# Kernel tuning notes

Hardware: AMD Instinct MI355X
Metric: run time of the kernel (lower is better)

## Reference

```python
import jax, jax.numpy as jnp
import numpy as np

N_GENES = 2048   # col_dim: nodes of the PPI graph, feature dim of cols-SAGE
N_CELLS = 4096   # row_dim: nodes of the KNN graph, feature dim of rows-SAGE
E_KNN = 61440
E_PPI = 65536
INTER = 512
EMBD = 128
SLOPE = 0.01       # LeakyReLU default negative_slope
SCALE_PARAM = 3.0  # cols_encoder custom attention scale

_PARAM_SHAPES = [
    ("c0_wl", (N_GENES, N_GENES)), ("c0_wr", (N_GENES, N_GENES)), ("c0_b", (N_GENES,)),
    ("r0_wl", (N_CELLS, N_CELLS)), ("r0_wr", (N_CELLS, N_CELLS)), ("r0_b", (N_CELLS,)),
    ("c1_wl", (N_GENES, N_GENES)), ("c1_wr", (N_GENES, N_GENES)), ("c1_b", (N_GENES,)),
    ("r1_wl", (N_CELLS, N_CELLS)), ("r1_wr", (N_CELLS, N_CELLS)), ("r1_b", (N_CELLS,)),
    ("gr_w", (N_CELLS, INTER)), ("gr_b", (INTER,)),
    ("tr_wq", (INTER, EMBD)), ("tr_bq", (EMBD,)), ("tr_wk", (INTER, EMBD)), ("tr_bk", (EMBD,)),
    ("tr_wv", (INTER, EMBD)), ("tr_bv", (EMBD,)), ("tr_ws", (INTER, EMBD)), ("tr_bs", (EMBD,)),
    ("gc_w", (N_GENES, INTER)), ("gc_b", (INTER,)),
    ("tc_wq", (INTER, EMBD)), ("tc_bq", (EMBD,)), ("tc_wk", (INTER, EMBD)), ("tc_bk", (EMBD,)),
    ("tc_wv", (INTER, EMBD)), ("tc_bv", (EMBD,)), ("tc_ws", (INTER, EMBD)), ("tc_bs", (EMBD,)),
    ("d1_w", (EMBD, INTER)), ("d1_b", (INTER,)),
    ("d2_w", (INTER, INTER)), ("d2_b", (INTER,)),
    ("d3_w", (INTER, N_GENES)), ("d3_b", (N_GENES,)),
]


def setup_inputs() -> dict:
    key = jax.random.key(0)
    ki = iter(jax.random.split(key, 64))
    inp = {
        "x": jax.random.normal(next(ki), (N_GENES, N_CELLS), jnp.float32),
        "knn_edge_index": jax.random.randint(next(ki), (2, E_KNN), 0, N_CELLS, dtype=jnp.int32),
        "ppi_edge_index": jax.random.randint(next(ki), (2, E_PPI), 0, N_GENES, dtype=jnp.int32),
    }
    for name, shape in _PARAM_SHAPES:
        scale = 1.0 / float(np.sqrt(shape[0])) if len(shape) == 2 else 0.01
        inp[name] = jax.random.normal(next(ki), shape, jnp.float32) * scale
    return inp


def _leaky(x):
    return jax.nn.leaky_relu(x, SLOPE)


def _gcn(x, ei, w, b):
    # GCNConv: add self loops, symmetric D^-1/2 (A+I) D^-1/2 normalization
    n = x.shape[0]
    loop = jnp.arange(n, dtype=ei.dtype)
    src = jnp.concatenate([ei[0], loop])
    dst = jnp.concatenate([ei[1], loop])
    deg = jax.ops.segment_sum(jnp.ones(src.shape, x.dtype), dst, n)
    dinv = jnp.where(deg > 0, jax.lax.rsqrt(jnp.maximum(deg, 1.0)), 0.0)
    h = x @ w
    msg = h[src] * (dinv[src] * dinv[dst])[:, None]
    return jax.ops.segment_sum(msg, dst, n) + b


def _sage(x, ei, wl, wr, b):
    # SAGEConv: mean neighbor aggregation -> lin_l, plus root lin_r
    n = x.shape[0]
    src, dst = ei[0], ei[1]
    s = jax.ops.segment_sum(x[src], dst, n)
    cnt = jax.ops.segment_sum(jnp.ones(src.shape, x.dtype), dst, n)
    agg = s / jnp.maximum(cnt, 1.0)[:, None]
    return agg @ wl + x @ wr + b


def _tconv(x, ei, wq, bq, wk, bk, wv, bv, ws, bs, scale_param):
    # TransformerConv (heads=1). scale_param=None -> per-target softmax;
    # otherwise the custom mean/std standardization + sigmoid (TransformerConvReducrLayer).
    n, d = x.shape[0], wq.shape[1]
    q = x @ wq + bq
    k = x @ wk + bk
    v = x @ wv + bv
    src, dst = ei[0], ei[1]
    alpha = jnp.sum(q[dst] * k[src], axis=-1) / jnp.sqrt(jnp.asarray(d, x.dtype))
    if scale_param is None:
        m = jax.ops.segment_max(alpha, dst, n)
        e = jnp.exp(alpha - m[dst])
        z = jax.ops.segment_sum(e, dst, n)
        a = e / jnp.where(z > 0, z, 1.0)[dst]
    else:
        mu = jnp.mean(alpha)
        sd = jnp.std(alpha, ddof=1)  # torch.std is unbiased
        a = jax.nn.sigmoid((alpha - mu) / ((1.0 / scale_param) * sd))
    out = jax.ops.segment_sum(a[:, None] * v[src], dst, n)
    return out + x @ ws + bs  # root skip (lin_skip)


def reference(x, knn_edge_index, ppi_edge_index,
              c0_wl, c0_wr, c0_b, r0_wl, r0_wr, r0_b,
              c1_wl, c1_wr, c1_b, r1_wl, r1_wr, r1_b,
              gr_w, gr_b, tr_wq, tr_bq, tr_wk, tr_bk, tr_wv, tr_bv, tr_ws, tr_bs,
              gc_w, gc_b, tc_wq, tc_bq, tc_wk, tc_bk, tc_wv, tc_bv, tc_ws, tc_bs,
              d1_w, d1_b, d2_w, d2_b, d3_w, d3_b):
    # dropout layers are identity at inference
    emb = x  # [genes, cells]
    for (cwl, cwr, cb, rwl, rwr, rb) in [
        (c0_wl, c0_wr, c0_b, r0_wl, r0_wr, r0_b),
        (c1_wl, c1_wr, c1_b, r1_wl, r1_wr, r1_b),
    ]:
        emb = _leaky(_sage(emb.T, knn_edge_index, cwl, cwr, cb)).T  # cells graph
        emb = _leaky(_sage(emb, ppi_edge_index, rwl, rwr, rb))      # genes graph
    # rows encoder: GCN + TransformerConv (softmax attention) over PPI graph
    hr = _leaky(_gcn(emb, ppi_edge_index, gr_w, gr_b))
    emb_rows = _tconv(hr, ppi_edge_index, tr_wq, tr_bq, tr_wk, tr_bk,
                      tr_wv, tr_bv, tr_ws, tr_bs, None)
    # cols encoder: GCN + reducer TransformerConv (sigmoid-standardized attention) over KNN graph
    hc = _leaky(_gcn(emb.T, knn_edge_index, gc_w, gc_b))
    emb_cols = _tconv(hc, knn_edge_index, tc_wq, tc_bq, tc_wk, tc_bk,
                      tc_wv, tc_bv, tc_ws, tc_bs, SCALE_PARAM)
    # feature decoder MLP
    h = jax.nn.relu(emb_cols @ d1_w + d1_b)
    h = jax.nn.relu(h @ d2_w + d2_b)
    out_features = h @ d3_w + d3_b
    return (emb_rows, emb_cols, out_features)
```

## Files before the change

kernel.cpp:

```cpp
#include <hip/hip_runtime.h>
#include <math.h>

#define NG 2048
#define NC 4096
#define EKNN 61440
#define EPPI 65536

typedef __attribute__((ext_vector_type(8))) short short8v;
typedef __attribute__((ext_vector_type(4))) float f32x4;
typedef unsigned short ushort_t;

static inline int cdiv(int a, int b) { return (a + b - 1) / b; }

__device__ __forceinline__ unsigned short f2b(float f) {
    union { float f; unsigned int i; } v; v.f = f;
    unsigned int r = v.i + 0x7FFFu + ((v.i >> 16) & 1u);
    return (unsigned short)(r >> 16);
}
__device__ __forceinline__ float bl(unsigned int u) { union { unsigned int i; float f; } v; v.i = u << 16; return v.f; }
__device__ __forceinline__ float bh(unsigned int u) { union { unsigned int i; float f; } v; v.i = u & 0xFFFF0000u; return v.f; }
__device__ __forceinline__ unsigned int pk2(float a, float b) { return (unsigned int)f2b(a) | ((unsigned int)f2b(b) << 16); }

__device__ __forceinline__ int xcd_swz_id() {
    const int nwg = gridDim.x * gridDim.y;
    const int orig = blockIdx.y * gridDim.x + blockIdx.x;
    const int q = nwg >> 3, r = nwg & 7;
    const int xcd = orig & 7, off = orig >> 3;
    return (xcd < r ? xcd * (q + 1) : r * (q + 1) + (xcd - r) * q) + off;
}

#define GLOAD_LDS16(gp, lp) __builtin_amdgcn_global_load_lds( \
    (const __attribute__((address_space(1))) void*)(gp),      \
    (__attribute__((address_space(3))) void*)(lp), 16, 0, 0)

template<int ACT, bool BIAS, bool OBF>
__global__ __launch_bounds__(256)
void gemm_bf16(const ushort_t* __restrict__ A,
               const ushort_t* __restrict__ Bt,
               const float* __restrict__ bias,
               float* __restrict__ Cf, ushort_t* __restrict__ Cb,
               int M, int N, int K) {
    __shared__ ushort_t lds[2][2][128 * 32];
    const int tid = threadIdx.x;
    const int lane = tid & 63, wv = tid >> 6;
    const int wm = wv >> 1, wn = wv & 1;
    const int swzid = xcd_swz_id();
    const int bm = (swzid / gridDim.x) << 7, bn = (swzid % gridDim.x) << 7;

    const ushort_t* gA = A + (size_t)bm * K;
    const ushort_t* gB = Bt + (size_t)bn * K;
    const int rsub = lane >> 2;
    const int qsw  = (lane & 3) ^ ((lane >> 3) & 3);
    const int KT = K >> 5;

    f32x4 acc[4][4];
    #pragma unroll
    for (int i = 0; i < 4; ++i)
        #pragma unroll
        for (int j = 0; j < 4; ++j) acc[i][j] = (f32x4){0.f, 0.f, 0.f, 0.f};

    auto stage = [&](int buf, int k0) {
        #pragma unroll
        for (int t = 0; t < 2; ++t) {
            const int br = (wv * 2 + t) * 16;
            GLOAD_LDS16(gA + (size_t)(br + rsub) * K + k0 + qsw * 8, &lds[buf][0][br * 32]);
            GLOAD_LDS16(gB + (size_t)(br + rsub) * K + k0 + qsw * 8, &lds[buf][1][br * 32]);
        }
    };
    const int rl = lane & 15, kg = lane >> 4;
    const int swr = (kg ^ ((rl >> 1) & 3)) * 8;

    stage(0, 0);
    int buf = 0;
    for (int kt = 0; kt < KT; ++kt) {
        __syncthreads();
        if (kt + 1 < KT) stage(buf ^ 1, (kt + 1) << 5);
        short8v a[4], b[4];
        #pragma unroll
        for (int mi = 0; mi < 4; ++mi)
            a[mi] = *(const short8v*)&lds[buf][0][(wm * 64 + mi * 16 + rl) * 32 + swr];
        #pragma unroll
        for (int ni = 0; ni < 4; ++ni)
            b[ni] = *(const short8v*)&lds[buf][1][(wn * 64 + ni * 16 + rl) * 32 + swr];
        #pragma unroll
        for (int mi = 0; mi < 4; ++mi)
            #pragma unroll
            for (int ni = 0; ni < 4; ++ni)
                acc[mi][ni] = __builtin_amdgcn_mfma_f32_16x16x32_bf16(a[mi], b[ni], acc[mi][ni], 0, 0, 0);
        buf ^= 1;
    }
    const int colL = lane & 15, rq = lane >> 4;
    #pragma unroll
    for (int mi = 0; mi < 4; ++mi) {
        const int row0 = bm + wm * 64 + mi * 16 + rq * 4;
        #pragma unroll
        for (int ni = 0; ni < 4; ++ni) {
            const int col = bn + wn * 64 + ni * 16 + colL;
            float bv = 0.f;
            if (BIAS) bv = bias[col];
            #pragma unroll
            for (int r = 0; r < 4; ++r) {
                const size_t off = (size_t)(row0 + r) * N + col;
                float v = acc[mi][ni][r];
                if (BIAS) v += bv;
                if (ACT == 2) v = fmaxf(v, 0.f);
                if (OBF) Cb[off] = f2b(v); else Cf[off] = v;
            }
        }
    }
}

template<bool BIAS, bool OBF>
__global__ __launch_bounds__(256)
void gemm2_bf16(const ushort_t* __restrict__ A0, const ushort_t* __restrict__ Bt0,
                const float* __restrict__ bias0, float* __restrict__ Cf0, ushort_t* __restrict__ Cb0,
                int N0, int K0, int nx0, int nb0,
// ... 80 lines not shown
}

__global__ __launch_bounds__(256)
void gemm_sage(const ushort_t* __restrict__ A0, const ushort_t* __restrict__ B0t,
               const ushort_t* __restrict__ A1, const ushort_t* __restrict__ B1t,
               const float* __restrict__ bias, ushort_t* __restrict__ Cb,
               int M, int N, int K) {
    __shared__ ushort_t lds[2][2][128 * 32];
    const int tid = threadIdx.x;
    const int lane = tid & 63, wv = tid >> 6;
    const int wm = wv >> 1, wn = wv & 1;
    const int swzid = xcd_swz_id();
    const int bm = (swzid / gridDim.x) << 7, bn = (swzid % gridDim.x) << 7;

    const ushort_t* gA0 = A0 + (size_t)bm * K;
    const ushort_t* gB0 = B0t + (size_t)bn * K;
    const ushort_t* gA1 = A1 + (size_t)bm * K;
    const ushort_t* gB1 = B1t + (size_t)bn * K;
    const int rsub = lane >> 2;
    const int qsw  = (lane & 3) ^ ((lane >> 3) & 3);
    const int KT = K >> 5;

    f32x4 acc[4][4];
    #pragma unroll
    for (int i = 0; i < 4; ++i)
        #pragma unroll
        for (int j = 0; j < 4; ++j) acc[i][j] = (f32x4){0.f, 0.f, 0.f, 0.f};

    auto stage = [&](int buf, int kt) {
        const int half = kt >= KT;
        const int k0 = (half ? (kt - KT) : kt) << 5;
        const ushort_t* sA = half ? gA1 : gA0;
        const ushort_t* sB = half ? gB1 : gB0;
        #pragma unroll
        for (int t = 0; t < 2; ++t) {
            const int br = (wv * 2 + t) * 16;
            GLOAD_LDS16(sA + (size_t)(br + rsub) * K + k0 + qsw * 8, &lds[buf][0][br * 32]);
            GLOAD_LDS16(sB + (size_t)(br + rsub) * K + k0 + qsw * 8, &lds[buf][1][br * 32]);
        }
    };
    const int rl = lane & 15, kg = lane >> 4;
    const int swr = (kg ^ ((rl >> 1) & 3)) * 8;

    stage(0, 0);
    int buf = 0;
    const int KT2 = KT * 2;
    for (int kt = 0; kt < KT2; ++kt) {
        __syncthreads();
        if (kt + 1 < KT2) stage(buf ^ 1, kt + 1);
        short8v a[4], b[4];
        #pragma unroll
        for (int mi = 0; mi < 4; ++mi)
            a[mi] = *(const short8v*)&lds[buf][0][(wm * 64 + mi * 16 + rl) * 32 + swr];
        #pragma unroll
        for (int ni = 0; ni < 4; ++ni)
            b[ni] = *(const short8v*)&lds[buf][1][(wn * 64 + ni * 16 + rl) * 32 + swr];
        #pragma unroll
        for (int mi = 0; mi < 4; ++mi)
            #pragma unroll
            for (int ni = 0; ni < 4; ++ni)
                acc[mi][ni] = __builtin_amdgcn_mfma_f32_16x16x32_bf16(a[mi], b[ni], acc[mi][ni], 0, 0, 0);
        buf ^= 1;
    }
    const int colL = lane & 15, rq = lane >> 4;
    #pragma unroll
    for (int mi = 0; mi < 4; ++mi) {
        const int row0 = bm + wm * 64 + mi * 16 + rq * 4;
        float bz[4];
        #pragma unroll
        for (int r = 0; r < 4; ++r) bz[r] = bias[row0 + r];
        #pragma unroll
        for (int ni = 0; ni < 4; ++ni) {
            const int col = bn + wn * 64 + ni * 16 + colL;
            #pragma unroll
            for (int r = 0; r < 4; ++r) {
                float v = acc[mi][ni][r] + bz[r];
                v = v > 0.f ? v : 0.01f * v;
                Cb[(size_t)(row0 + r) * N + col] = f2b(v);
            }
        }
    }
}

__global__ __launch_bounds__(256)
void transpose_f2b(const float* __restrict__ in, ushort_t* __restrict__ out, int R, int C) {
    __shared__ ushort_t t[64][65];
    const int bx = blockIdx.x << 6, by = blockIdx.y << 6;
    const int tr = threadIdx.x >> 4;
    const int tc = (threadIdx.x & 15) << 2;
    #pragma unroll
    for (int i = 0; i < 4; ++i) {
        const int rr = tr + i * 16;
        const float4 v = *(const float4*)(in + (size_t)(by + rr) * C + bx + tc);
        t[rr][tc + 0] = f2b(v.x); t[rr][tc + 1] = f2b(v.y);
        t[rr][tc + 2] = f2b(v.z); t[rr][tc + 3] = f2b(v.w);
    }
    __syncthreads();
    #pragma unroll
    for (int i = 0; i < 4; ++i) {
        const int cc = tr + i * 16;
        ushort4 o;
        o.x = t[tc + 0][cc]; o.y = t[tc + 1][cc];
        o.z = t[tc + 2][cc]; o.w = t[tc + 3][cc];
        *(ushort4*)(out + (size_t)(bx + cc) * R + by + tc) = o;
    }
}

__global__ __launch_bounds__(256)
void transpose_f2b2(const float* __restrict__ in0, ushort_t* __restrict__ out0,
                    const float* __restrict__ in1, ushort_t* __restrict__ out1, int R, int C) {
    const float* in = blockIdx.z ? in1 : in0;
    ushort_t* out = blockIdx.z ? out1 : out0;
    __shared__ ushort_t t[64][65];
    const int bx = blockIdx.x << 6, by = blockIdx.y << 6;
    const int tr = threadIdx.x >> 4;
    const int tc = (threadIdx.x & 15) << 2;
    #pragma unroll
    for (int i = 0; i < 4; ++i) {
        const int rr = tr + i * 16;
        const float4 v = *(const float4*)(in + (size_t)(by + rr) * C + bx + tc);
        t[rr][tc + 0] = f2b(v.x); t[rr][tc + 1] = f2b(v.y);
        t[rr][tc + 2] = f2b(v.z); t[rr][tc + 3] = f2b(v.w);
    }
    __syncthreads();
    #pragma unroll
    for (int i = 0; i < 4; ++i) {
        const int cc = tr + i * 16;
        ushort4 o;
        o.x = t[tc + 0][cc]; o.y = t[tc + 1][cc];
        o.z = t[tc + 2][cc]; o.w = t[tc + 3][cc];
        *(ushort4*)(out + (size_t)(bx + cc) * R + by + tc) = o;
    }
}

__global__ __launch_bounds__(256)
void transpose_b2b(const ushort_t* __restrict__ in, ushort_t* __restrict__ out, int R, int C) {
    __shared__ ushort_t t[64][65];
    const int bx = blockIdx.x << 6, by = blockIdx.y << 6;
    const int tr = threadIdx.x >> 4;
    const int tc = (threadIdx.x & 15) << 2;
    #pragma unroll
    for (int i = 0; i < 4; ++i) {
        const int rr = tr + i * 16;
        const ushort4 v = *(const ushort4*)(in + (size_t)(by + rr) * C + bx + tc);
        t[rr][tc + 0] = v.x; t[rr][tc + 1] = v.y;
        t[rr][tc + 2] = v.z; t[rr][tc + 3] = v.w;
    }
    __syncthreads();
    #pragma unroll
    for (int i = 0; i < 4; ++i) {
        const int cc = tr + i * 16;
        ushort4 o;
        o.x = t[tc + 0][cc]; o.y = t[tc + 1][cc];
        o.z = t[tc + 2][cc]; o.w = t[tc + 3][cc];
        *(ushort4*)(out + (size_t)(bx + cc) * R + by + tc) = o;
    }
}

__global__ __launch_bounds__(256)
void transpose_qkvs8(const float* __restrict__ w0, const float* __restrict__ w1,
                     const float* __restrict__ w2, const float* __restrict__ w3,
                     const float* __restrict__ w4, const float* __restrict__ w5,
                     const float* __restrict__ w6, const float* __restrict__ w7,
                     ushort_t* __restrict__ outR, ushort_t* __restrict__ outC) {
    const int z = blockIdx.z;
    const float* in;
    switch (z) {
        case 0: in = w0; break; case 1: in = w1; break;
        case 2: in = w2; break; case 3: in = w3; break;
        case 4: in = w4; break; case 5: in = w5; break;
        case 6: in = w6; break; default: in = w7; break;
    }
    ushort_t* o = (z < 4 ? outR + (size_t)z * 128 * 512 : outC + (size_t)(z - 4) * 128 * 512);
    __shared__ ushort_t t[64][65];
    const int bx = blockIdx.x << 6, by = blockIdx.y << 6;
    const int tr = threadIdx.x >> 4;
    const int tc = (threadIdx.x & 15) << 2;
    #pragma unroll
    for (int i = 0; i < 4; ++i) {
        const int rr = tr + i * 16;
        const float4 v = *(const float4*)(in + (size_t)(by + rr) * 128 + bx + tc);
        t[rr][tc + 0] = f2b(v.x); t[rr][tc + 1] = f2b(v.y);
        t[rr][tc + 2] = f2b(v.z); t[rr][tc + 3] = f2b(v.w);
    }
    __syncthreads();
    #pragma unroll
    for (int i = 0; i < 4; ++i) {
        const int cc = tr + i * 16;
        ushort4 ov;
        ov.x = t[tc + 0][cc]; ov.y = t[tc + 1][cc];
        ov.z = t[tc + 2][cc]; ov.w = t[tc + 3][cc];
        *(ushort4*)(o + (size_t)(bx + cc) * 512 + by + tc) = ov;
    }
}

__global__ void count_dst2(const int* __restrict__ pdst, float* __restrict__ cntp,
                           const int* __restrict__ kdst, float* __restrict__ cntk) {
    int e = blockIdx.x * blockDim.x + threadIdx.x;
    if (e < EPPI) atomicAdd(&cntp[pdst[e]], 1.0f);
    else if (e < EPPI + EKNN) atomicAdd(&cntk[kdst[e - EPPI]], 1.0f);
}

__global__ void make_dinv2(const float* __restrict__ cntp, float* __restrict__ dinvp,
                           const float* __restrict__ cntk, float* __restrict__ dinvk) {
    int i = blockIdx.x * blockDim.x + threadIdx.x;
    if (i < NG) dinvp[i] = rsqrtf(cntp[i] + 1.0f);
    else if (i < NG + NC) dinvk[i - NG] = rsqrtf(cntk[i - NG] + 1.0f);
}

__global__ __launch_bounds__(256)
void scan_rowptr2(const float* __restrict__ cntp, int* __restrict__ rpp,
                  const float* __restrict__ cntk, int* __restrict__ rpk) {
    const float* cnt = blockIdx.x ? cntk : cntp;
    int* rowptr = blockIdx.x ? rpk : rpp;
    const int n = blockIdx.x ? NC : NG;
    __shared__ int part[257];
    const int tid = threadIdx.x;
    const int per = n >> 8;
    const int base = tid * per;
    int s = 0;
    for (int i = 0; i < per; ++i) s += (int)cnt[base + i];
    part[tid + 1] = s;
    if (tid == 0) part[0] = 0;
    __syncthreads();
    if (tid == 0)
        for (int i = 1; i <= 256; ++i) part[i] += part[i - 1];
    __syncthreads();
    int run = part[tid];
    for (int i = 0; i < per; ++i) {
        rowptr[base + i] = run;
        run += (int)cnt[base + i];
    }
    if (tid == 255) rowptr[n] = run;
}

__global__ void fill_csr2(const int* __restrict__ psrc, const int* __restrict__ pdst,
                          const int* __restrict__ rpp, int* __restrict__ curp,
                          int* __restrict__ srcp, int* __restrict__ eidp,
                          const int* __restrict__ ksrc, const int* __restrict__ kdst,
                          const int* __restrict__ rpk, int* __restrict__ curk,
                          int* __restrict__ srck, int* __restrict__ eidk) {
    int e = blockIdx.x * blockDim.x + threadIdx.x;
    if (e < EPPI) {
        int d = pdst[e];
        int p = atomicAdd(&curp[d], 1);
        srcp[rpp[d] + p] = psrc[e];
        eidp[rpp[d] + p] = e;
    } else if (e < EPPI + EKNN) {
        int e2 = e - EPPI;
        int d = kdst[e2];
        int p = atomicAdd(&curk[d], 1);
        srck[rpk[d] + p] = ksrc[e2];
        eidk[rpk[d] + p] = e2;
    }
}

__global__ void concat8(const float* __restrict__ a, const float* __restrict__ b,
                        const float* __restrict__ c, const float* __restrict__ d,
                        const float* __restrict__ e, const float* __restrict__ f,
                        const float* __restrict__ g, const float* __restrict__ h,
                        float* __restrict__ o) {
    int i = threadIdx.x + blockIdx.x * blockDim.x;
    if (i >= 1024) return;
    const float* s;
    int j = i & 127;
    switch (i >> 7) {
        case 0: s = a; break; case 1: s = b; break; case 2: s = c; break; case 3: s = d; break;
        case 4: s = e; break; case 5: s = f; break; case 6: s = g; break; default: s = h; break;
    }
    o[i] = s[j];
}

template<int NS>
__global__ __launch_bounds__(256)
void sage_gather_b(const int* __restrict__ rowptr, const int* __restrict__ srcs,
                   const ushort_t* __restrict__ x, ushort_t* __restrict__ out) {
    const int F = NS * 2048;
    const int node = blockIdx.x, tid = threadIdx.x;
    const int beg = rowptr[node], end = rowptr[node + 1];
    __shared__ int snb[256];
    float acc[NS][8];
    #pragma unroll
    for (int s = 0; s < NS; ++s)
        #pragma unroll
        for (int j = 0; j < 8; ++j) acc[s][j] = 0.f;
    for (int c = beg; c < end; c += 256) {
        const int m = min(256, end - c);
        __syncthreads();
        if (tid < m) snb[tid] = srcs[c + tid];
        __syncthreads();
        #pragma unroll 2
        for (int i = 0; i < m; ++i) {
            const uint4* row = (const uint4*)(x + (size_t)snb[i] * F);
            #pragma unroll
            for (int s = 0; s < NS; ++s) {
                const uint4 v = row[tid + s * 256];
                acc[s][0] += bl(v.x); acc[s][1] += bh(v.x);
                acc[s][2] += bl(v.y); acc[s][3] += bh(v.y);
                acc[s][4] += bl(v.z); acc[s][5] += bh(v.z);
                acc[s][6] += bl(v.w); acc[s][7] += bh(v.w);
            }
        }
    }
    const float inv = 1.f / fmaxf((float)(end - beg), 1.f);
    uint4* orow = (uint4*)(out + (size_t)node * F);
    #pragma unroll
    for (int s = 0; s < NS; ++s) {
        uint4 o;
        o.x = pk2(acc[s][0] * inv, acc[s][1] * inv);
        o.y = pk2(acc[s][2] * inv, acc[s][3] * inv);
        o.z = pk2(acc[s][4] * inv, acc[s][5] * inv);
        o.w = pk2(acc[s][6] * inv, acc[s][7] * inv);
        orow[tid + s * 256] = o;
    }
}

__global__ __launch_bounds__(128)
void gcn_gather2(const int* __restrict__ rpp, const int* __restrict__ srcp,
                 const ushort_t* __restrict__ hr, const float* __restrict__ dinvp,
                 const float* __restrict__ br, ushort_t* __restrict__ outr,
                 const int* __restrict__ rpk, const int* __restrict__ srck,
                 const ushort_t* __restrict__ hc, const float* __restrict__ dinvk,
                 const float* __restrict__ bc, ushort_t* __restrict__ outc) {
    const bool cols = blockIdx.x >= NG;
    const int node = cols ? blockIdx.x - NG : blockIdx.x;
    const int tid = threadIdx.x;
    const int* rowptr = cols ? rpk : rpp;
    const int* srcs = cols ? srck : srcp;
    const ushort_t* h = cols ? hc : hr;
    const float* dinv = cols ? dinvk : dinvp;
    const float* b = cols ? bc : br;
    ushort_t* out = cols ? outc : outr;

    const int beg = rowptr[node], end = rowptr[node + 1];
    __shared__ int snb[128];
    __shared__ float sdi[128];
    float ax = 0.f, ay = 0.f, az = 0.f, aw = 0.f;
    for (int c = beg; c < end; c += 128) {
        const int m = min(128, end - c);
        __syncthreads();
        if (tid < m) { int s = srcs[c + tid]; snb[tid] = s; sdi[tid] = dinv[s]; }
        __syncthreads();
        for (int i = 0; i < m; ++i) {
            const uint2 v = ((const uint2*)(h + (size_t)snb[i] * 512))[tid];
            const float w = sdi[i];
            ax += bl(v.x) * w; ay += bh(v.x) * w;
            az += bl(v.y) * w; aw += bh(v.y) * w;
        }
    }
    const float dd = dinv[node];
    const uint2 hv = ((const uint2*)(h + (size_t)node * 512))[tid];
    const float4 bv = ((const float4*)b)[tid];
    float4 o;
    o.x = ax * dd + bl(hv.x) * dd * dd + bv.x;
    o.y = ay * dd + bh(hv.x) * dd * dd + bv.y;
    o.z = az * dd + bl(hv.y) * dd * dd + bv.z;
    o.w = aw * dd + bh(hv.y) * dd * dd + bv.w;
    o.x = o.x > 0.f ? o.x : 0.01f * o.x;
    o.y = o.y > 0.f ? o.y : 0.01f * o.y;
    o.z = o.z > 0.f ? o.z : 0.01f * o.z;
    o.w = o.w > 0.f ? o.w : 0.01f * o.w;
    ((uint2*)(out + (size_t)node * 512))[tid] = make_uint2(pk2(o.x, o.y), pk2(o.z, o.w));
}

__global__ __launch_bounds__(256)
void edge_dot2(const int* __restrict__ psrc, const int* __restrict__ pdst,
               const float* __restrict__ qr, float* __restrict__ alphap,
               const int* __restrict__ ksrc, const int* __restrict__ kdst,
               const float* __restrict__ qc, float* __restrict__ alphak) {
    int wid = (blockIdx.x * blockDim.x + threadIdx.x) >> 6;
    int lane = threadIdx.x & 63;
    const float* q;
    float* out;
    int s, d, w;
    if (wid < EPPI) {
        w = wid; s = psrc[w]; d = pdst[w]; q = qr; out = alphap;
    } else if (wid < EPPI + EKNN) {
        w = wid - EPPI; s = ksrc[w]; d = kdst[w]; q = qc; out = alphak;
    } else return;
    const size_t qb = (size_t)d * 512;
    const size_t kb = (size_t)s * 512 + 128;
    float v = q[qb + lane] * q[kb + lane] + q[qb + 64 + lane] * q[kb + 64 + lane];
    #pragma unroll
    for (int off = 32; off; off >>= 1) v += __shfl_down(v, off);
    if (lane == 0) out[w] = v * 0.08838834764831845f;
}

__global__ __launch_bounds__(256)
void reduce_stats(const float* __restrict__ a, int E, double* __restrict__ stats) {
    double s = 0.0, s2 = 0.0;
    for (int i = blockIdx.x * blockDim.x + threadIdx.x; i < E; i += gridDim.x * blockDim.x) {
        double x = a[i];
        s += x; s2 += x * x;
    }
    #pragma unroll
    for (int off = 32; off; off >>= 1) {
        s += __shfl_down(s, off);
        s2 += __shfl_down(s2, off);
    }
    __shared__ double sh[4][2];
    int w = threadIdx.x >> 6;
    if ((threadIdx.x & 63) == 0) { sh[w][0] = s; sh[w][1] = s2; }
    __syncthreads();
    if (threadIdx.x == 0) {
        double t = sh[0][0] + sh[1][0] + sh[2][0] + sh[3][0];
        double t2 = sh[0][1] + sh[1][1] + sh[2][1] + sh[3][1];
        atomicAdd(&stats[0], t);
        atomicAdd(&stats[1], t2);
    }
}

__global__ __launch_bounds__(128)
void tconv2(const int* __restrict__ rpp, const int* __restrict__ srcp,
            const int* __restrict__ eidp, const float* __restrict__ alphap,
            const float* __restrict__ qr, float* __restrict__ outr,
            const int* __restrict__ rpk, const int* __restrict__ srck,
            const int* __restrict__ eidk, const float* __restrict__ alphak,
            const float* __restrict__ qc, const double* __restrict__ stats,
            float* __restrict__ outc, ushort_t* __restrict__ ob) {
    const int tid = threadIdx.x;
    __shared__ int snb[128];
    __shared__ float sa[128];
    if (blockIdx.x < NG) {
        const int node = blockIdx.x;
        const int beg = rpp[node], end = rpp[node + 1];
        float mx = -INFINITY;
        for (int c = beg; c < end; c += 128) {
            const int m = min(128, end - c);
            __syncthreads();
            if (tid < m) sa[tid] = alphap[eidp[c + tid]];
            __syncthreads();
            for (int i = 0; i < m; ++i) mx = fmaxf(mx, sa[i]);
        }
        float acc = 0.f, z = 0.f;
        for (int c = beg; c < end; c += 128) {
            const int m = min(128, end - c);
            __syncthreads();
            if (tid < m) { snb[tid] = srcp[c + tid]; sa[tid] = __expf(alphap[eidp[c + tid]] - mx); }
            __syncthreads();
            for (int i = 0; i < m; ++i) {
                z += sa[i];
                acc += sa[i] * qr[(size_t)snb[i] * 512 + 256 + tid];
            }
        }
        const float r = acc * (z > 0.f ? 1.f / z : 0.f) + qr[(size_t)node * 512 + 384 + tid];
        outr[(size_t)node * 128 + tid] = r;
    } else {
        const int node = blockIdx.x - NG;
        const int beg = rpk[node], end = rpk[node + 1];
        const double sum = stats[0], sumsq = stats[1];
        const double mu = sum / (double)EKNN;
        const double var = (sumsq - sum * sum / (double)EKNN) / (double)(EKNN - 1);
        const float sd = (float)sqrt(fmax(var, 0.0));
        const float kk = 3.0f / sd;
        const float fmu = (float)mu;
        float acc = 0.f;
        for (int c = beg; c < end; c += 128) {
            const int m = min(128, end - c);
            __syncthreads();
            if (tid < m) {
                snb[tid] = srck[c + tid];
                const float t = (alphak[eidk[c + tid]] - fmu) * kk;
                sa[tid] = 1.f / (1.f + __expf(-t));
            }
            __syncthreads();
            for (int i = 0; i < m; ++i)
                acc += sa[i] * qc[(size_t)snb[i] * 512 + 256 + tid];
        }
        const float r = acc + qc[(size_t)node * 512 + 384 + tid];
        outc[(size_t)node * 128 + tid] = r;
        ob[(size_t)node * 128 + tid] = f2b(r);
    }
}

static constexpr size_t NBIG = (size_t)NG * NC;
static constexpr size_t NBH = NBIG / 2;
static constexpr size_t OFF_B1 = 0;
static constexpr size_t OFF_B2 = NBH;
static constexpr size_t OFF_B3 = 2 * NBH;
static constexpr size_t OFF_WBF = 3 * NBH;
static constexpr size_t OFF_OV   = OFF_WBF + 2097152;
static constexpr size_t OFF_HRB  = OFF_OV;
static constexpr size_t OFF_HCB  = OFF_HRB + 524288;
static constexpr size_t OFF_H2B  = OFF_HCB + 1048576;
static constexpr size_t OFF_H3B  = OFF_H2B + 524288;
static constexpr size_t OFF_QKVSR = OFF_H3B + 1048576;
static constexpr size_t OFF_QKVSC = OFF_QKVSR + 1048576;
static constexpr size_t OFF_CBF  = OFF_QKVSC + 2097152;
static constexpr size_t OFF_WQR  = OFF_CBF + 262144;
static constexpr size_t OFF_WQC  = OFF_WQR + 131072;
static constexpr size_t OFF_D1T  = OFF_WQC + 131072;
static constexpr size_t OFF_D2T  = OFF_D1T + 32768;
static constexpr size_t OFF_D3T  = OFF_D2T + 131072;
static constexpr size_t OFF_TAIL = OFF_WBF + 2 * NBIG;
static constexpr size_t OFF_B4   = OFF_TAIL;
static constexpr size_t OFF_ALPHAP = OFF_B4 + 1024;
static constexpr size_t OFF_ALPHAK = OFF_ALPHAP + EPPI;
static constexpr size_t OFF_CNT  = OFF_ALPHAK + EKNN;
static constexpr size_t OFF_DINVP = OFF_CNT + 12288;
static constexpr size_t OFF_DINVK = OFF_DINVP + NG;
static constexpr size_t OFF_STATS = OFF_DINVK + NC;
static constexpr size_t OFF_RPP  = OFF_STATS + 16;
static constexpr size_t OFF_RPK  = OFF_RPP + 2064;
static constexpr size_t OFF_SRCP = OFF_RPK + 4112;
static constexpr size_t OFF_EIDP = OFF_SRCP + EPPI;
static constexpr size_t OFF_SRCK = OFF_EIDP + EPPI;
static constexpr size_t OFF_EIDK = OFF_SRCK + EKNN;

extern "C" void kernel_launch(void* const* d_in, const int* in_sizes, int n_in,
                              void* d_out, int out_size, void* d_ws, size_t ws_size,
                              hipStream_t stream) {
    const float* x      = (const float*)d_in[0];
    const int*   knn    = (const int*)d_in[1];
    const int*   ppi    = (const int*)d_in[2];
    const float* c0_wl = (const float*)d_in[3],  *c0_wr = (const float*)d_in[4],  *c0_b = (const float*)d_in[5];
    const float* r0_wl = (const float*)d_in[6],  *r0_wr = (const float*)d_in[7],  *r0_b = (const float*)d_in[8];
    const float* c1_wl = (const float*)d_in[9],  *c1_wr = (const float*)d_in[10], *c1_b = (const float*)d_in[11];
    const float* r1_wl = (const float*)d_in[12], *r1_wr = (const float*)d_in[13], *r1_b = (const float*)d_in[14];
    const float* gr_w  = (const float*)d_in[15], *gr_b  = (const float*)d_in[16];
    const float* tr_wq = (const float*)d_in[17], *tr_bq = (const float*)d_in[18];
    const float* tr_wk = (const float*)d_in[19], *tr_bk = (const float*)d_in[20];
    const float* tr_wv = (const float*)d_in[21], *tr_bv = (const float*)d_in[22];
    const float* tr_ws = (const float*)d_in[23], *tr_bs = (const float*)d_in[24];
    const float* gc_w  = (const float*)d_in[25], *gc_b  = (const float*)d_in[26];
    const float* tc_wq = (const float*)d_in[27], *tc_bq = (const float*)d_in[28];
    const float* tc_wk = (const float*)d_in[29], *tc_bk = (const float*)d_in[30];
    const float* tc_wv = (const float*)d_in[31], *tc_bv = (const float*)d_in[32];
    const float* tc_ws = (const float*)d_in[33], *tc_bs = (const float*)d_in[34];
    const float* d1_w  = (const float*)d_in[35], *d1_b  = (const float*)d_in[36];
    const float* d2_w  = (const float*)d_in[37], *d2_b  = (const float*)d_in[38];
    const float* d3_w  = (const float*)d_in[39], *d3_b  = (const float*)d_in[40];

    const int* knn_src = knn, *knn_dst = knn + EKNN;
    const int* ppi_src = ppi, *ppi_dst = ppi + EPPI;

    float* ws = (float*)d_ws;
    ushort_t* B1 = (ushort_t*)(ws + OFF_B1);
    ushort_t* B2 = (ushort_t*)(ws + OFF_B2);
    ushort_t* B3 = (ushort_t*)(ws + OFF_B3);
    ushort_t* WBF0 = (ushort_t*)(ws + OFF_WBF);
    ushort_t* WBF1 = WBF0 + 2 * NBIG;
    ushort_t* GRT = WBF0;
    ushort_t* GCT = WBF0 + 2097152;
    ushort_t* HRB = (ushort_t*)(ws + OFF_HRB);
    ushort_t* HCB = (ushort_t*)(ws + OFF_HCB);
    ushort_t* H2B = (ushort_t*)(ws + OFF_H2B);
    ushort_t* H3B = (ushort_t*)(ws + OFF_H3B);
    float* QKVSR = ws + OFF_QKVSR;
    float* QKVSC = ws + OFF_QKVSC;
    ushort_t* CBF = (ushort_t*)(ws + OFF_CBF);
    ushort_t* WQR = (ushort_t*)(ws + OFF_WQR);
    ushort_t* WQC = (ushort_t*)(ws + OFF_WQC);
    ushort_t* D1T = (ushort_t*)(ws + OFF_D1T);
    ushort_t* D2T = (ushort_t*)(ws + OFF_D2T);
    ushort_t* D3T = (ushort_t*)(ws + OFF_D3T);
    float* B4 = ws + OFF_B4;
    float* ALPHAP = ws + OFF_ALPHAP;
    float* ALPHAK = ws + OFF_ALPHAK;
    float* CNTP = ws + OFF_CNT;
    float* CNTK = CNTP + NG;
    int* CURP = (int*)(CNTK + NC);
    int* CURK = CURP + NG;
    float* DINVP = ws + OFF_DINVP;
    float* DINVK = ws + OFF_DINVK;
    double* STATS = (double*)(ws + OFF_STATS);
    int* RPP  = (int*)(ws + OFF_RPP);
    int* RPK  = (int*)(ws + OFF_RPK);
    int* SRCP = (int*)(ws + OFF_SRCP);
    int* EIDP = (int*)(ws + OFF_EIDP);
    int* SRCK = (int*)(ws + OFF_SRCK);
    int* EIDK = (int*)(ws + OFF_EIDK);

    float* out_rows = (float*)d_out;
    float* out_cols = out_rows + (size_t)NG * 128;
    float* out_feat = out_cols + (size_t)NC * 128;

    auto tW = [&](const float* Wsrc, int K, int N, ushort_t* dst) {
        transpose_f2b<<<dim3(N >> 6, K >> 6), 256, 0, stream>>>(Wsrc, dst, K, N);
    };
    auto gemm = [&](const ushort_t* Abf, const ushort_t* Wt, const float* bias,
                    float* Cf, ushort_t* Cb, int M, int N, int K, int mode) {
        dim3 g(N >> 7, M >> 7), blk(256);
        switch (mode) {
            case 2: gemm_bf16<0, true,  false><<<g, blk, 0, stream>>>(Abf, Wt, bias, Cf, nullptr, M, N, K); break;
            case 3: gemm_bf16<2, true,  true ><<<g, blk, 0, stream>>>(Abf, Wt, bias, nullptr, Cb, M, N, K); break;
        }
    };

    hipMemsetAsync(CNTP, 0, 12288 * 4, stream);
    count_dst2<<<cdiv(EPPI + EKNN, 256), 256, 0, stream>>>(ppi_dst, CNTP, knn_dst, CNTK);
    make_dinv2<<<cdiv(NG + NC, 256), 256, 0, stream>>>(CNTP, DINVP, CNTK, DINVK);
    scan_rowptr2<<<2, 256, 0, stream>>>(CNTP, RPP, CNTK, RPK);
    fill_csr2<<<cdiv(EPPI + EKNN, 256), 256, 0, stream>>>(ppi_src, ppi_dst, RPP, CURP, SRCP, EIDP,
                                                          knn_src, knn_dst, RPK, CURK, SRCK, EIDK);

    transpose_f2b<<<dim3(NC >> 6, NG >> 6), 256, 0, stream>>>(x, B1, NG, NC);
    const float* cwl[2] = {c0_wl, c1_wl}; const float* cwr[2] = {c0_wr, c1_wr}; const float* cbb[2] = {c0_b, c1_b};
    const float* rwl[2] = {r0_wl, r1_wl}; const float* rwr[2] = {r0_wr, r1_wr}; const float* rbb[2] = {r0_b, r1_b};
    for (int l = 0; l < 2; ++l) {
        sage_gather_b<1><<<NC, 256, 0, stream>>>(RPK, SRCK, B1, B2);
        transpose_f2b2<<<dim3(NG >> 6, NG >> 6, 2), 256, 0, stream>>>(cwl[l], WBF0, cwr[l], WBF1, NG, NG);
        gemm_sage<<<dim3(NC >> 7, NG >> 7), 256, 0, stream>>>(WBF0, B2, WBF1, B1, cbb[l], B3, NG, NC, NG);
        sage_gather_b<2><<<NG, 256, 0, stream>>>(RPP, SRCP, B3, B2);
        transpose_f2b2<<<dim3(NC >> 6, NC >> 6, 2), 256, 0, stream>>>(rwl[l], WBF0, rwr[l], WBF1, NC, NC);
        gemm_sage<<<dim3(NG >> 7, NC >> 7), 256, 0, stream>>>(WBF0, B2, WBF1, B3, rbb[l], B1, NC, NG, NC);
    }
    transpose_b2b<<<dim3(NG >> 6, NC >> 6), 256, 0, stream>>>(B1, B3, NC, NG);

    tW(gr_w, NC, 512, GRT);
    tW(gc_w, NG, 512, GCT);
    gemm2_bf16<false, true><<<64 + 128, 256, 0, stream>>>(
        B3, GRT, nullptr, nullptr, HRB, 512, NC, 4, 64,
        B1, GCT, nullptr, nullptr, HCB, 512, NG, 4);
    gcn_gather2<<<NG + NC, 128, 0, stream>>>(RPP, SRCP, HRB, DINVP, gr_b, H2B,
                                             RPK, SRCK, HCB, DINVK, gc_b, H3B);
    transpose_qkvs8<<<dim3(2, 8, 8), 256, 0, stream>>>(tr_wq, tr_wk, tr_wv, tr_ws,
                                                       tc_wq, tc_wk, tc_wv, tc_ws, WQR, WQC);
    concat8<<<4, 256, 0, stream>>>(tr_bq, tr_bk, tr_bv, tr_bs, tc_bq, tc_bk, tc_bv, tc_bs, B4);
    gemm2_bf16<true, false><<<64 + 128, 256, 0, stream>>>(
        H2B, WQR, B4, QKVSR, nullptr, 512, 512, 4, 64,
        H3B, WQC, B4 + 512, QKVSC, nullptr, 512, 512, 4);
    edge_dot2<<<cdiv((EPPI + EKNN) * 64, 256), 256, 0, stream>>>(
        ppi_src, ppi_dst, QKVSR, ALPHAP, knn_src, knn_dst, QKVSC, ALPHAK);
    hipMemsetAsync(STATS, 0, 16, stream);
    reduce_stats<<<256, 256, 0, stream>>>(ALPHAK, EKNN, STATS);
    tconv2<<<NG + NC, 128, 0, stream>>>(RPP, SRCP, EIDP, ALPHAP, QKVSR, out_rows,
                                        RPK, SRCK, EIDK, ALPHAK, QKVSC, STATS, out_cols, CBF);

    tW(d1_w, 128, 512, D1T);
    gemm(CBF, D1T, d1_b, nullptr, H2B, NC, 512, 128, 3);
    tW(d2_w, 512, 512, D2T);
    gemm(H2B, D2T, d2_b, nullptr, H3B, NC, 512, 512, 3);
    tW(d3_w, 512, NG, D3T);
    gemm(H3B, D3T, d3_b, out_feat, nullptr, NC, NG, 512, 2);

    (void)in_sizes; (void)n_in; (void)out_size; (void)ws_size;
}
```

Baseline: 974.8 us.

## Fuse neighbor gathers with weight transposes into one multi-job kernel launch

Adds a gather_tr kernel whose first blocks do the SAGE mean-gather and whose remaining blocks run a table of transpose/convert jobs passed by value. It merges each gather with its weight transposes and folds all post-loop weight transposes into one launch. It also zeroes the stats buffer inside concat8 instead of using a memset. The aim is fewer launches and overlap of the gather with transpose work, at the cost of a linear job lookup per block and a workspace layout that must not overlap the big weight buffers.

After: 943.7 us. -3.2%, faster.

```diff
diff --git a/kernel.cpp b/kernel.cpp
--- a/kernel.cpp
+++ b/kernel.cpp
@@ -5,6 +5,7 @@
 #define NC 4096
 #define EKNN 61440
 #define EPPI 65536
+#define NJMAX 14
 
 typedef __attribute__((ext_vector_type(8))) short short8v;
 typedef __attribute__((ext_vector_type(4))) float f32x4;
@@ -32,6 +33,14 @@
 #define GLOAD_LDS16(gp, lp) __builtin_amdgcn_global_load_lds( \
     (const __attribute__((address_space(1))) void*)(gp),      \
     (__attribute__((address_space(3))) void*)(lp), 16, 0, 0)
+
+struct TJobs {
+    const void* in[NJMAX];
+    ushort_t* out[NJMAX];
+    int R[NJMAX], C[NJMAX], start[NJMAX], type[NJMAX];
+    int n;
+    int nGather;
+};
 
 template<int ACT, bool BIAS, bool OBF>
 __global__ __launch_bounds__(256)
@@ -278,6 +287,93 @@
     }
 }
 
+template<int NS>
+__global__ __launch_bounds__(256)
+void gather_tr(const int* __restrict__ rowptr, const int* __restrict__ srcs,
+               const ushort_t* __restrict__ x, ushort_t* __restrict__ xout,
+               TJobs jobs) {
+    __shared__ ushort_t shm[64 * 65];
+    const int tid = threadIdx.x;
+    if ((int)blockIdx.x < jobs.nGather) {
+        const int F = NS * 2048;
+        const int node = blockIdx.x;
+        int* snb = (int*)shm;
+        const int beg = rowptr[node], end = rowptr[node + 1];
+        float acc[NS][8];
+        #pragma unroll
+        for (int s = 0; s < NS; ++s)
+            #pragma unroll
+            for (int j = 0; j < 8; ++j) acc[s][j] = 0.f;
+        for (int c = beg; c < end; c += 256) {
+            const int m = min(256, end - c);
+            __syncthreads();
+            if (tid < m) snb[tid] = srcs[c + tid];
+            __syncthreads();
+            #pragma unroll 2
+            for (int i = 0; i < m; ++i) {
+                const uint4* row = (const uint4*)(x + (size_t)snb[i] * F);
+                #pragma unroll
+                for (int s = 0; s < NS; ++s) {
+                    const uint4 v = row[tid + s * 256];
+                    acc[s][0] += bl(v.x); acc[s][1] += bh(v.x);
+                    acc[s][2] += bl(v.y); acc[s][3] += bh(v.y);
+                    acc[s][4] += bl(v.z); acc[s][5] += bh(v.z);
+                    acc[s][6] += bl(v.w); acc[s][7] += bh(v.w);
+                }
+            }
+        }
+        const float inv = 1.f / fmaxf((float)(end - beg), 1.f);
+        uint4* orow = (uint4*)(xout + (size_t)node * F);
+        #pragma unroll
+        for (int s = 0; s < NS; ++s) {
+            uint4 o;
+            o.x = pk2(acc[s][0] * inv, acc[s][1] * inv);
+            o.y = pk2(acc[s][2] * inv, acc[s][3] * inv);
+            o.z = pk2(acc[s][4] * inv, acc[s][5] * inv);
+            o.w = pk2(acc[s][6] * inv, acc[s][7] * inv);
+            orow[tid + s * 256] = o;
+        }
+        return;
+    }
+    int b = blockIdx.x - jobs.nGather;
+    int j = 0;
+    while (j + 1 < jobs.n && b >= jobs.start[j + 1]) ++j;
+    const int t = b - jobs.start[j];
+    const int R = jobs.R[j], C = jobs.C[j];
+    const int nx = C >> 6;
+    const int bx = (t % nx) << 6, by = (t / nx) << 6;
+    const int tr = tid >> 4, tc = (tid & 15) << 2;
+    if (jobs.type[j] == 0) {
+        const float* in = (const float*)jobs.in[j];
+        #pragma unroll
+        for (int i = 0; i < 4; ++i) {
+            const int rr = tr + i * 16;
+            const float4 v = *(const float4*)(in + (size_t)(by + rr) * C + bx + tc);
+            shm[rr * 65 + tc + 0] = f2b(v.x); shm[rr * 65 + tc + 1] = f2b(v.y);
+            shm[rr * 65 + tc + 2] = f2b(v.z); shm[rr * 65 + tc + 3] = f2b(v.w);
+        }
+    } else {
+        const ushort_t* in = (const ushort_t*)jobs.in[j];
+        #pragma unroll
+        for (int i = 0; i < 4; ++i) {
+            const int rr = tr + i * 16;
+            const ushort4 v = *(const ushort4*)(in + (size_t)(by + rr) * C + bx + tc);
+            shm[rr * 65 + tc + 0] = v.x; shm[rr * 65 + tc + 1] = v.y;
+            shm[rr * 65 + tc + 2] = v.z; shm[rr * 65 + tc + 3] = v.w;
+        }
+    }
+    __syncthreads();
+    ushort_t* out = jobs.out[j];
+    #pragma unroll
+    for (int i = 0; i < 4; ++i) {
+        const int cc = tr + i * 16;
+        ushort4 o;
+        o.x = shm[(tc + 0) * 65 + cc]; o.y = shm[(tc + 1) * 65 + cc];
+        o.z = shm[(tc + 2) * 65 + cc]; o.w = shm[(tc + 3) * 65 + cc];
+        *(ushort4*)(out + (size_t)(bx + cc) * R + by + tc) = o;
+    }
+}
+
 __global__ __launch_bounds__(256)
 void transpose_f2b(const float* __restrict__ in, ushort_t* __restrict__ out, int R, int C) {
     __shared__ ushort_t t[64][65];
@@ -299,94 +395,6 @@
         o.x = t[tc + 0][cc]; o.y = t[tc + 1][cc];
         o.z = t[tc + 2][cc]; o.w = t[tc + 3][cc];
         *(ushort4*)(out + (size_t)(bx + cc) * R + by + tc) = o;
-    }
-}
-
-__global__ __launch_bounds__(256)
-void transpose_f2b2(const float* __restrict__ in0, ushort_t* __restrict__ out0,
-                    const float* __restrict__ in1, ushort_t* __restrict__ out1, int R, int C) {
-    const float* in = blockIdx.z ? in1 : in0;
-    ushort_t* out = blockIdx.z ? out1 : out0;
-    __shared__ ushort_t t[64][65];
-    const int bx = blockIdx.x << 6, by = blockIdx.y << 6;
-    const int tr = threadIdx.x >> 4;
-    const int tc = (threadIdx.x & 15) << 2;
-    #pragma unroll
-    for (int i = 0; i < 4; ++i) {
-        const int rr = tr + i * 16;
-        const float4 v = *(const float4*)(in + (size_t)(by + rr) * C + bx + tc);
-        t[rr][tc + 0] = f2b(v.x); t[rr][tc + 1] = f2b(v.y);
-        t[rr][tc + 2] = f2b(v.z); t[rr][tc + 3] = f2b(v.w);
-    }
-    __syncthreads();
-    #pragma unroll
-    for (int i = 0; i < 4; ++i) {
-        const int cc = tr + i * 16;
-        ushort4 o;
-        o.x = t[tc + 0][cc]; o.y = t[tc + 1][cc];
-        o.z = t[tc + 2][cc]; o.w = t[tc + 3][cc];
-        *(ushort4*)(out + (size_t)(bx + cc) * R + by + tc) = o;
-    }
-}
-
-__global__ __launch_bounds__(256)
-void transpose_b2b(const ushort_t* __restrict__ in, ushort_t* __restrict__ out, int R, int C) {
-    __shared__ ushort_t t[64][65];
-    const int bx = blockIdx.x << 6, by = blockIdx.y << 6;
-    const int tr = threadIdx.x >> 4;
-    const int tc = (threadIdx.x & 15) << 2;
-    #pragma unroll
-    for (int i = 0; i < 4; ++i) {
-        const int rr = tr + i * 16;
-        const ushort4 v = *(const ushort4*)(in + (size_t)(by + rr) * C + bx + tc);
-        t[rr][tc + 0] = v.x; t[rr][tc + 1] = v.y;
-        t[rr][tc + 2] = v.z; t[rr][tc + 3] = v.w;
-    }
-    __syncthreads();
-    #pragma unroll
-    for (int i = 0; i < 4; ++i) {
-        const int cc = tr + i * 16;
-        ushort4 o;
-        o.x = t[tc + 0][cc]; o.y = t[tc + 1][cc];
-        o.z = t[tc + 2][cc]; o.w = t[tc + 3][cc];
-        *(ushort4*)(out + (size_t)(bx + cc) * R + by + tc) = o;
-    }
-}
-
-__global__ __launch_bounds__(256)
-void transpose_qkvs8(const float* __restrict__ w0, const float* __restrict__ w1,
-                     const float* __restrict__ w2, const float* __restrict__ w3,
-                     const float* __restrict__ w4, const float* __restrict__ w5,
-                     const float* __restrict__ w6, const float* __restrict__ w7,
-                     ushort_t* __restrict__ outR, ushort_t* __restrict__ outC) {
-    const int z = blockIdx.z;
-    const float* in;
-    switch (z) {
-        case 0: in = w0; break; case 1: in = w1; break;
-        case 2: in = w2; break; case 3: in = w3; break;
-        case 4: in = w4; break; case 5: in = w5; break;
-        case 6: in = w6; break; default: in = w7; break;
-    }
-    ushort_t* o = (z < 4 ? outR + (size_t)z * 128 * 512 : outC + (size_t)(z - 4) * 128 * 512);
-    __shared__ ushort_t t[64][65];
-    const int bx = blockIdx.x << 6, by = blockIdx.y << 6;
-    const int tr = threadIdx.x >> 4;
-    const int tc = (threadIdx.x & 15) << 2;
-    #pragma unroll
-    for (int i = 0; i < 4; ++i) {
-        const int rr = tr + i * 16;
-        const float4 v = *(const float4*)(in + (size_t)(by + rr) * 128 + bx + tc);
-        t[rr][tc + 0] = f2b(v.x); t[rr][tc + 1] = f2b(v.y);
-        t[rr][tc + 2] = f2b(v.z); t[rr][tc + 3] = f2b(v.w);
-    }
-    __syncthreads();
-    #pragma unroll
-    for (int i = 0; i < 4; ++i) {
-        const int cc = tr + i * 16;
-        ushort4 ov;
-        ov.x = t[tc + 0][cc]; ov.y = t[tc + 1][cc];
-        ov.z = t[tc + 2][cc]; ov.w = t[tc + 3][cc];
-        *(ushort4*)(o + (size_t)(bx + cc) * 512 + by + tc) = ov;
     }
 }
 
@@ -455,9 +463,10 @@
                         const float* __restrict__ c, const float* __restrict__ d,
                         const float* __restrict__ e, const float* __restrict__ f,
                         const float* __restrict__ g, const float* __restrict__ h,
-                        float* __restrict__ o) {
+                        float* __restrict__ o, double* __restrict__ stats) {
     int i = threadIdx.x + blockIdx.x * blockDim.x;
     if (i >= 1024) return;
+    if (i < 4) ((unsigned int*)stats)[i] = 0u;
     const float* s;
     int j = i & 127;
     switch (i >> 7) {
@@ -465,50 +474,6 @@
         case 4: s = e; break; case 5: s = f; break; case 6: s = g; break; default: s = h; break;
     }
     o[i] = s[j];
-}
-
-template<int NS>
-__global__ __launch_bounds__(256)
-void sage_gather_b(const int* __restrict__ rowptr, const int* __restrict__ srcs,
-                   const ushort_t* __restrict__ x, ushort_t* __restrict__ out) {
-    const int F = NS * 2048;
-    const int node = blockIdx.x, tid = threadIdx.x;
-    const int beg = rowptr[node], end = rowptr[node + 1];
-    __shared__ int snb[256];
-    float acc[NS][8];
-    #pragma unroll
-    for (int s = 0; s < NS; ++s)
-        #pragma unroll
-        for (int j = 0; j < 8; ++j) acc[s][j] = 0.f;
-    for (int c = beg; c < end; c += 256) {
-        const int m = min(256, end - c);
-        __syncthreads();
-        if (tid < m) snb[tid] = srcs[c + tid];
-        __syncthreads();
-        #pragma unroll 2
-        for (int i = 0; i < m; ++i) {
-            const uint4* row = (const uint4*)(x + (size_t)snb[i] * F);
-            #pragma unroll
-            for (int s = 0; s < NS; ++s) {
-                const uint4 v = row[tid + s * 256];
-                acc[s][0] += bl(v.x); acc[s][1] += bh(v.x);
-                acc[s][2] += bl(v.y); acc[s][3] += bh(v.y);
-                acc[s][4] += bl(v.z); acc[s][5] += bh(v.z);
-                acc[s][6] += bl(v.w); acc[s][7] += bh(v.w);
-            }
-        }
-    }
-    const float inv = 1.f / fmaxf((float)(end - beg), 1.f);
-    uint4* orow = (uint4*)(out + (size_t)node * F);
-    #pragma unroll
-    for (int s = 0; s < NS; ++s) {
-        uint4 o;
-        o.x = pk2(acc[s][0] * inv, acc[s][1] * inv);
-        o.y = pk2(acc[s][2] * inv, acc[s][3] * inv);
-        o.z = pk2(acc[s][4] * inv, acc[s][5] * inv);
-        o.w = pk2(acc[s][6] * inv, acc[s][7] * inv);
-        orow[tid + s * 256] = o;
-    }
 }
 
 __global__ __launch_bounds__(128)
@@ -675,19 +640,20 @@
 static constexpr size_t OFF_B2 = NBH;
 static constexpr size_t OFF_B3 = 2 * NBH;
 static constexpr size_t OFF_WBF = 3 * NBH;
-static constexpr size_t OFF_OV   = OFF_WBF + 2097152;
-static constexpr size_t OFF_HRB  = OFF_OV;
-static constexpr size_t OFF_HCB  = OFF_HRB + 524288;
-static constexpr size_t OFF_H2B  = OFF_HCB + 1048576;
-static constexpr size_t OFF_H3B  = OFF_H2B + 524288;
+static constexpr size_t OFF_GRT   = OFF_WBF;
+static constexpr size_t OFF_GCT   = OFF_GRT + 1048576;
+static constexpr size_t OFF_WQR   = OFF_GCT + 524288;
+static constexpr size_t OFF_WQC   = OFF_WQR + 131072;
+static constexpr size_t OFF_D1T   = OFF_WQC + 131072;
+static constexpr size_t OFF_D2T   = OFF_D1T + 32768;
+static constexpr size_t OFF_D3T   = OFF_D2T + 131072;
+static constexpr size_t OFF_HRB   = OFF_D3T + 524288;
+static constexpr size_t OFF_HCB   = OFF_HRB + 524288;
+static constexpr size_t OFF_H2B   = OFF_HCB + 1048576;
+static constexpr size_t OFF_H3B   = OFF_H2B + 524288;
 static constexpr size_t OFF_QKVSR = OFF_H3B + 1048576;
 static constexpr size_t OFF_QKVSC = OFF_QKVSR + 1048576;
-static constexpr size_t OFF_CBF  = OFF_QKVSC + 2097152;
-static constexpr size_t OFF_WQR  = OFF_CBF + 262144;
-static constexpr size_t OFF_WQC  = OFF_WQR + 131072;
-static constexpr size_t OFF_D1T  = OFF_WQC + 131072;
-static constexpr size_t OFF_D2T  = OFF_D1T + 32768;
-static constexpr size_t OFF_D3T  = OFF_D2T + 131072;
+static constexpr size_t OFF_CBF   = OFF_QKVSC + 2097152;
 static constexpr size_t OFF_TAIL = OFF_WBF + 2 * NBIG;
 static constexpr size_t OFF_B4   = OFF_TAIL;
 static constexpr size_t OFF_ALPHAP = OFF_B4 + 1024;
@@ -736,8 +702,13 @@
     ushort_t* B3 = (ushort_t*)(ws + OFF_B3);
     ushort_t* WBF0 = (ushort_t*)(ws + OFF_WBF);
     ushort_t* WBF1 = WBF0 + 2 * NBIG;
-    ushort_t* GRT = WBF0;
-    ushort_t* GCT = WBF0 + 2097152;
+    ushort_t* GRT = (ushort_t*)(ws + OFF_GRT);
+    ushort_t* GCT = (ushort_t*)(ws + OFF_GCT);
+    ushort_t* WQR = (ushort_t*)(ws + OFF_WQR);
+    ushort_t* WQC = (ushort_t*)(ws + OFF_WQC);
+    ushort_t* D1T = (ushort_t*)(ws + OFF_D1T);
+    ushort_t* D2T = (ushort_t*)(ws + OFF_D2T);
+    ushort_t* D3T = (ushort_t*)(ws + OFF_D3T);
     ushort_t* HRB = (ushort_t*)(ws + OFF_HRB);
     ushort_t* HCB = (ushort_t*)(ws + OFF_HCB);
     ushort_t* H2B = (ushort_t*)(ws + OFF_H2B);
@@ -745,21 +716,16 @@
     float* QKVSR = ws + OFF_QKVSR;
     float* QKVSC = ws + OFF_QKVSC;
     ushort_t* CBF = (ushort_t*)(ws + OFF_CBF);
-    ushort_t* WQR = (ushort_t*)(ws + OFF_WQR);
-    ushort_t* WQC = (ushort_t*)(ws + OFF_WQC);
-    ushort_t* D1T = (ushort_t*)(ws + OFF_D1T);
-    ushort_t* D2T = (ushort_t*)(ws + OFF_D2T);
-    ushort_t* D3T = (ushort_t*)(ws + OFF_D3T);
     float* B4 = ws + OFF_B4;
     float* ALPHAP = ws + OFF_ALPHAP;
     float* ALPHAK = ws + OFF_ALPHAK;
     float* CNTP = ws + OFF_CNT;
     float* CNTK = CNTP + NG;
-    int* CURP = (int*)(CNTK + NC);
-    int* CURK = CURP + NG;
     float* DINVP = ws + OFF_DINVP;
     float* DINVK = ws + OFF_DINVK;
     double* STATS = (double*)(ws + OFF_STATS);
+    int* CURP = (int*)(CNTK + NC);
+    int* CURK = CURP + NG;
     int* RPP  = (int*)(ws + OFF_RPP);
     int* RPK  = (int*)(ws + OFF_RPK);
     int* SRCP = (int*)(ws + OFF_SRCP);
@@ -771,15 +737,21 @@
     float* out_cols = out_rows + (size_t)NG * 128;
     float* out_feat = out_cols + (size_t)NC * 128;
 
-    auto tW = [&](const float* Wsrc, int K, int N, ushort_t* dst) {
-        transpose_f2b<<<dim3(N >> 6, K >> 6), 256, 0, stream>>>(Wsrc, dst, K, N);
+    auto addJ = [](TJobs& J, const void* in, ushort_t* out, int R, int C, int type) {
+        int k = J.n;
+        int prevEnd = (k == 0) ? 0 : J.start[k - 1] + (J.C[k - 1] >> 6) * (J.R[k - 1] >> 6);
+        J.in[k] = in; J.out[k] = out; J.R[k] = R; J.C[k] = C; J.type[k] = type;
+        J.start[k] = prevEnd; J.n = k + 1;
+    };
+    auto jBlocks = [](const TJobs& J) {
+        return (J.n == 0) ? 0 : J.start[J.n - 1] + (J.C[J.n - 1] >> 6) * (J.R[J.n - 1] >> 6);
     };
     auto gemm = [&](const ushort_t* Abf, const ushort_t* Wt, const float* bias,
                     float* Cf, ushort_t* Cb, int M, int N, int K, int mode) {
         dim3 g(N >> 7, M >> 7), blk(256);
         switch (mode) {
-            case 2: gemm_bf16<0, true,  false><<<g, blk, 0, stream>>>(Abf, Wt, bias, Cf, nullptr, M, N, K); break;
-            case 3: gemm_bf16<2, true,  true ><<<g, blk, 0, stream>>>(Abf, Wt, bias, nullptr, Cb, M, N, K); break;
+            case 2: gemm_bf16<0, true, false><<<g, blk, 0, stream>>>(Abf, Wt, bias, Cf, nullptr, M, N, K); break;
+            case 3: gemm_bf16<2, true, true ><<<g, blk, 0, stream>>>(Abf, Wt, bias, nullptr, Cb, M, N, K); break;
         }
     };
 
@@ -794,40 +766,54 @@
     const float* cwl[2] = {c0_wl, c1_wl}; const float* cwr[2] = {c0_wr, c1_wr}; const float* cbb[2] = {c0_b, c1_b};
     const float* rwl[2] = {r0_wl, r1_wl}; const float* rwr[2] = {r0_wr, r1_wr}; const float* rbb[2] = {r0_b, r1_b};
     for (int l = 0; l < 2; ++l) {
-        sage_gather_b<1><<<NC, 256, 0, stream>>>(RPK, SRCK, B1, B2);
-        transpose_f2b2<<<dim3(NG >> 6, NG >> 6, 2), 256, 0, stream>>>(cwl[l], WBF0, cwr[l], WBF1, NG, NG);
+        TJobs Jc{}; Jc.n = 0; Jc.nGather = NC;
+        addJ(Jc, cwl[l], WBF0, NG, NG, 0);
+        addJ(Jc, cwr[l], WBF1, NG, NG, 0);
+        gather_tr<1><<<NC + jBlocks(Jc), 256, 0, stream>>>(RPK, SRCK, B1, B2, Jc);
         gemm_sage<<<dim3(NC >> 7, NG >> 7), 256, 0, stream>>>(WBF0, B2, WBF1, B1, cbb[l], B3, NG, NC, NG);
-        sage_gather_b<2><<<NG, 256, 0, stream>>>(RPP, SRCP, B3, B2);
-        transpose_f2b2<<<dim3(NC >> 6, NC >> 6, 2), 256, 0, stream>>>(rwl[l], WBF0, rwr[l], WBF1, NC, NC);
+        TJobs Jr{}; Jr.n = 0; Jr.nGather = NG;
+        addJ(Jr, rwl[l], WBF0, NC, NC, 0);
+        addJ(Jr, rwr[l], WBF1, NC, NC, 0);
+        gather_tr<2><<<NG + jBlocks(Jr), 256, 0, stream>>>(RPP, SRCP, B3, B2, Jr);
         gemm_sage<<<dim3(NG >> 7, NC >> 7), 256, 0, stream>>>(WBF0, B2, WBF1, B3, rbb[l], B1, NC, NG, NC);
     }
-    transpose_b2b<<<dim3(NG >> 6, NC >> 6), 256, 0, stream>>>(B1, B3, NC, NG);
-
-    tW(gr_w, NC, 512, GRT);
-    tW(gc_w, NG, 512, GCT);
+
+    {
+        TJobs Jp{}; Jp.n = 0; Jp.nGather = 0;
+        addJ(Jp, B1, B3, NC, NG, 1);
+        addJ(Jp, gr_w, GRT, NC, 512, 0);
+        addJ(Jp, gc_w, GCT, NG, 512, 0);
+        addJ(Jp, tr_wq, WQR + 0 * 65536, 512, 128, 0);
+        addJ(Jp, tr_wk, WQR + 1 * 65536, 512, 128, 0);
+        addJ(Jp, tr_wv, WQR + 2 * 65536, 512, 128, 0);
+        addJ(Jp, tr_ws, WQR + 3 * 65536, 512, 128, 0);
+        addJ(Jp, tc_wq, WQC + 0 * 65536, 512, 128, 0);
+        addJ(Jp, tc_wk, WQC + 1 * 65536, 512, 128, 0);
+        addJ(Jp, tc_wv, WQC + 2 * 65536, 512, 128, 0);
+        addJ(Jp, tc_ws, WQC + 3 * 65536, 512, 128, 0);
+        addJ(Jp, d1_w, D1T, 128, 512, 0);
+        addJ(Jp, d2_w, D2T, 512, 512, 0);
+        addJ(Jp, d3_w, D3T, 512, NG, 0);
+        gather_tr<1><<<jBlocks(Jp), 256, 0, stream>>>(RPK, SRCK, B1, B2, Jp);
+    }
+
     gemm2_bf16<false, true><<<64 + 128, 256, 0, stream>>>(
         B3, GRT, nullptr, nullptr, HRB, 512, NC, 4, 64,
         B1, GCT, nullptr, nullptr, HCB, 512, NG, 4);
     gcn_gather2<<<NG + NC, 128, 0, stream>>>(RPP, SRCP, HRB, DINVP, gr_b, H2B,
                                              RPK, SRCK, HCB, DINVK, gc_b, H3B);
-    transpose_qkvs8<<<dim3(2, 8, 8), 256, 0, stream>>>(tr_wq, tr_wk, tr_wv, tr_ws,
-                                                       tc_wq, tc_wk, tc_wv, tc_ws, WQR, WQC);
-    concat8<<<4, 256, 0, stream>>>(tr_bq, tr_bk, tr_bv, tr_bs, tc_bq, tc_bk, tc_bv, tc_bs, B4);
+    concat8<<<4, 256, 0, stream>>>(tr_bq, tr_bk, tr_bv, tr_bs, tc_bq, tc_bk, tc_bv, tc_bs, B4, STATS);
     gemm2_bf16<true, false><<<64 + 128, 256, 0, stream>>>(
         H2B, WQR, B4, QKVSR, nullptr, 512, 512, 4, 64,
         H3B, WQC, B4 + 512, QKVSC, nullptr, 512, 512, 4);
     edge_dot2<<<cdiv((EPPI + EKNN) * 64, 256), 256, 0, stream>>>(
         ppi_src, ppi_dst, QKVSR, ALPHAP, knn_src, knn_dst, QKVSC, ALPHAK);
-    hipMemsetAsync(STATS, 0, 16, stream);
     reduce_stats<<<256, 256, 0, stream>>>(ALPHAK, EKNN, STATS);
     tconv2<<<NG + NC, 128, 0, stream>>>(RPP, SRCP, EIDP, ALPHAP, QKVSR, out_rows,
                                         RPK, SRCK, EIDK, ALPHAK, QKVSC, STATS, out_cols, CBF);
 
-    tW(d1_w, 128, 512, D1T);
     gemm(CBF, D1T, d1_b, nullptr, H2B, NC, 512, 128, 3);
-    tW(d2_w, 512, 512, D2T);
     gemm(H2B, D2T, d2_b, nullptr, H3B, NC, 512, 512, 3);
-    tW(d3_w, 512, NG, D3T);
     gemm(H3B, D3T, d3_b, out_feat, nullptr, NC, NG, 512, 2);
 
     (void)in_sizes; (void)n_in; (void)out_size; (void)ws_size;
```
